# Optimization experiments

Measured on AMD Instinct MI355X. Metric: run time of the kernel, lower is better.

## Reference

```python
import jax, jax.numpy as jnp
import numpy as np

N, E = 50000, 800000
IN_DIM, HIDDEN, HEADS, OUT_DIM = 128, 64, 2, 128
NEG_SLOPE = 0.2


def setup_inputs() -> dict:
    key = jax.random.key(0)
    ks = jax.random.split(key, 12)
    s = lambda k, *sh: jax.random.normal(k, sh, dtype=jnp.float32) * (1.0 / np.sqrt(sh[0]))
    return {
        "x": jax.random.normal(ks[0], (N, IN_DIM), dtype=jnp.float32),
        "edge_index": jax.random.randint(ks[1], (2, E), 0, N, dtype=jnp.int64),
        # layer 1 (heads=2, concat=True)
        "Wl1": s(ks[2], IN_DIM, HEADS * HIDDEN),
        "Wr1": s(ks[3], IN_DIM, HEADS * HIDDEN),
        "att1": jax.random.normal(ks[4], (HEADS, HIDDEN), dtype=jnp.float32) * 0.1,
        "b1": jnp.zeros((HEADS * HIDDEN,), dtype=jnp.float32),
        # layer 2 (heads=1, concat=False -> mean)
        "Wl2": s(ks[5], HEADS * HIDDEN, OUT_DIM),
        "Wr2": s(ks[6], HEADS * HIDDEN, OUT_DIM),
        "att2": jax.random.normal(ks[7], (1, OUT_DIM), dtype=jnp.float32) * 0.1,
        "b2": jnp.zeros((OUT_DIM,), dtype=jnp.float32),
    }


def _gatv2_layer(x, src, dst, Wl, Wr, att, bias, heads, concat):
    n = x.shape[0]
    c = Wl.shape[1] // heads
    xl = (x @ Wl).reshape(n, heads, c)  # source transform
    xr = (x @ Wr).reshape(n, heads, c)  # target transform
    e = jax.nn.leaky_relu(xl[src] + xr[dst], NEG_SLOPE)      # (E, H, C)
    alpha = jnp.einsum("ehc,hc->eh", e, att)                 # (E, H)
    # softmax over incoming edges per destination node
    amax = jax.ops.segment_max(alpha, dst, num_segments=n)
    alpha = jnp.exp(alpha - amax[dst])
    denom = jax.ops.segment_sum(alpha, dst, num_segments=n)
    alpha = alpha / (denom[dst] + 1e-16)
    msg = xl[src] * alpha[:, :, None]                        # (E, H, C)
    out = jax.ops.segment_sum(msg, dst, num_segments=n)      # (N, H, C)
    out = out.reshape(n, heads * c) if concat else out.mean(axis=1)
    return out + bias


def reference(x, edge_index, Wl1, Wr1, att1, b1, Wl2, Wr2, att2, b2):
    n = x.shape[0]
    # PyG GATv2Conv default: add self loops
    loops = jnp.arange(n, dtype=edge_index.dtype)
    src = jnp.concatenate([edge_index[0], loops])
    dst = jnp.concatenate([edge_index[1], loops])
    h = jax.nn.elu(_gatv2_layer(x, src, dst, Wl1, Wr1, att1, b1, HEADS, True))
    h = jax.nn.elu(_gatv2_layer(h, src, dst, Wl2, Wr2, att2, b2, 1, False))
    return h
```

## Files before the change

### kernel.cpp

```cpp
#include <hip/hip_runtime.h>
#include <hip/hip_bf16.h>

#define N_NODES 50000
#define N_EDGES 800000
#define TOT_E   (N_EDGES + N_NODES)
#define NEG_SLOPE 0.2f
#define NBKT 98
#define CHUNK 4096
#define NCHUNK ((TOT_E + CHUNK - 1) / CHUNK)
#define BKT_CAP 12288

typedef __attribute__((ext_vector_type(8))) short bf16x8;
typedef __attribute__((ext_vector_type(4))) float f32x4;

static __device__ __forceinline__ unsigned short f2bf(float f) {
    unsigned int u = __float_as_uint(f);
    unsigned int r = (u + 0x7FFFu + ((u >> 16) & 1u)) >> 16;
    return (unsigned short)r;
}
static __device__ __forceinline__ float bf2f(unsigned short h) {
    return __uint_as_float(((unsigned int)h) << 16);
}
static __device__ __forceinline__ unsigned short f2h(float f) {
    _Float16 h = (_Float16)f;
    return __builtin_bit_cast(unsigned short, h);
}
static __device__ __forceinline__ float h2f(unsigned short u) {
    return (float)__builtin_bit_cast(_Float16, u);
}

__global__ __launch_bounds__(1024) void kA1(const int* __restrict__ dstp,
                                            int* __restrict__ bcount) {
    __shared__ int h[NBKT];
    int t = threadIdx.x;
    if (t < NBKT) h[t] = 0;
    __syncthreads();
    int base = blockIdx.x * CHUNK;
    int nloc = min(CHUNK, TOT_E - base);
    for (int i = t; i < nloc; i += 1024) {
        int e = base + i;
        int d = (e < N_EDGES) ? dstp[e] : (e - N_EDGES);
        atomicAdd(&h[d >> 9], 1);
    }
    __syncthreads();
    if (t < NBKT && h[t]) atomicAdd(&bcount[t], h[t]);
}

__global__ void kScan98(const int* __restrict__ bcount, int* __restrict__ bbase,
                        int* __restrict__ bcursor) {
    __shared__ int s[128];
    int t = threadIdx.x;
    int own = (t < NBKT) ? bcount[t] : 0;
    s[t] = own;
    __syncthreads();
    for (int off = 1; off < 128; off <<= 1) {
        int v = (t >= off) ? s[t - off] : 0;
        __syncthreads();
        s[t] += v;
        __syncthreads();
    }
    if (t < NBKT) {
        int base = s[t] - own;
        bbase[t] = base;
        bcursor[t] = base;
    }
    if (t == NBKT - 1) bbase[NBKT] = s[t];
}

__global__ __launch_bounds__(1024) void kA2(const int* __restrict__ srcp,
                                            const int* __restrict__ dstp,
                                            int* __restrict__ bcursor,
                                            unsigned* __restrict__ ebuf) {
    __shared__ int h[NBKT];
    __shared__ int lbase[NBKT];
    __shared__ int lcur[NBKT];
    __shared__ unsigned stage[CHUNK];
    int t = threadIdx.x;
    if (t < NBKT) h[t] = 0;
    __syncthreads();
    int base = blockIdx.x * CHUNK;
    int nloc = min(CHUNK, TOT_E - base);
    for (int i = t; i < nloc; i += 1024) {
        int e = base + i;
        int d = (e < N_EDGES) ? dstp[e] : (e - N_EDGES);
        atomicAdd(&h[d >> 9], 1);
    }
    __syncthreads();
    if (t < NBKT) lbase[t] = h[t] ? atomicAdd(&bcursor[t], h[t]) : 0;
    if (t == 0) {
        int run = 0;
        for (int b = 0; b < NBKT; ++b) { lcur[b] = run; run += h[b]; }
    }
    __syncthreads();
    for (int i = t; i < nloc; i += 1024) {
        int e = base + i;
        int d = (e < N_EDGES) ? dstp[e] : (e - N_EDGES);
        int s = (e < N_EDGES) ? srcp[e] : (e - N_EDGES);
        int b = d >> 9;
        int p = atomicAdd(&lcur[b], 1);
        stage[p] = (unsigned)s | ((unsigned)(d & 511) << 16) | ((unsigned)b << 25);
    }
    __syncthreads();
    for (int i = t; i < nloc; i += 1024) {
        unsigned v = stage[i];
        int b = v >> 25;
        int p = lbase[b] + i - (lcur[b] - h[b]);
        ebuf[p] = v & 0x1FFFFFFu;
    }
}

__global__ __launch_bounds__(1024) void kB(const unsigned* __restrict__ ebuf,
                                           const int* __restrict__ bbase,
                                           int* __restrict__ rowptr,
                                           int* __restrict__ esrc) {
    __shared__ int h[512];
    __shared__ int sc[512];
    __shared__ int st2[BKT_CAP];
    int b = blockIdx.x;
    int t = threadIdx.x;
    int gb = bbase[b];
    int cnt = bbase[b + 1] - gb;
    if (t < 512) h[t] = 0;
    __syncthreads();
    for (int i = t; i < cnt; i += 1024)
        atomicAdd(&h[(ebuf[gb + i] >> 16) & 511], 1);
    __syncthreads();
    if (t < 512) sc[t] = h[t];
    __syncthreads();
    for (int off = 1; off < 512; off <<= 1) {
        int v = (t < 512 && t >= off) ? sc[t - off] : 0;
        __syncthreads();
        if (t < 512) sc[t] += v;
        __syncthreads();
    }
    if (t < 512) h[t] = sc[t] - h[t];
    __syncthreads();
    int node0 = b << 9;
    if (t < 512) {
        int gn = node0 + t;
        if (gn < N_NODES) rowptr[gn] = gb + h[t];
    }
    if (b == NBKT - 1 && t == 0) rowptr[N_NODES] = TOT_E;
    for (int i = t; i < cnt; i += 1024) {
        unsigned v = ebuf[gb + i];
        int p = atomicAdd(&h[(v >> 16) & 511], 1);
        st2[p] = (int)(v & 0xFFFFu);
    }
    __syncthreads();
    for (int i = t; i < cnt; i += 1024) esrc[gb + i] = st2[i];
}

__global__ void k_pack(const float* __restrict__ Wa, const float* __restrict__ Wb,
                       unsigned short* __restrict__ Bp) {
    int idx = blockIdx.x * 256 + threadIdx.x;
    int j = idx & 7, lane = (idx >> 3) & 63, t = idx >> 9;
    int ks = t >> 4, ctg = t & 15;
    int k = (ks * 32 + (lane >> 4) * 8 + j) & 127;
    int n = ctg * 16 + (lane & 15);
    float v = (n < 128) ? Wa[k * 128 + n] : Wb[k * 128 + (n - 128)];
    Bp[idx] = f2bf(v);
}

template <bool F32IN>
__global__ __launch_bounds__(256) void k_mfma_lin(const void* __restrict__ Ain,
                                                  const unsigned short* __restrict__ Bp,
                                                  unsigned short* __restrict__ outA,
                                                  unsigned short* __restrict__ outB, int M) {
    __shared__ unsigned short lds_a[64][264];
    int tid = threadIdx.x;
    int n0 = blockIdx.x * 64;
    if (F32IN) {
        const float* X = (const float*)Ain;
#pragma unroll
        for (int r = 0; r < 8; ++r) {
            int c = r * 256 + tid;
            int row = c >> 5;
            int col4 = (c & 31) * 4;
            int gr = n0 + row;
            if (gr >= M) gr = M - 1;
            float4 v = *(const float4*)&X[(size_t)gr * 128 + col4];
            float vv[4] = {v.x, v.y, v.z, v.w};
            ushort4 hh, ll;
            unsigned short* hp = &hh.x;
            unsigned short* lp = &ll.x;
#pragma unroll
            for (int q = 0; q < 4; ++q) {
                unsigned short hv = f2bf(vv[q]);
                hp[q] = hv;
                lp[q] = f2bf(vv[q] - bf2f(hv));
            }
            *(ushort4*)&lds_a[row][col4] = hh;
            *(ushort4*)&lds_a[row][128 + col4] = ll;
        }
    } else {
        const unsigned short* Ap = (const unsigned short*)Ain;
#pragma unroll
        for (int r = 0; r < 8; ++r) {
            int c = r * 256 + tid;
            int row = c >> 5;
            int col = (c & 31) * 8;
            int gr = n0 + row;
            if (gr >= M) gr = M - 1;
            float4 v = *(const float4*)&Ap[(size_t)gr * 256 + col];
            *(float4*)&lds_a[row][col] = v;
        }
    }
    __syncthreads();

    int w = tid >> 6, lane = tid & 63;
    int lrow = lane & 15, lhi = lane >> 4;
    f32x4 acc[4][4] = {};
    const bf16x8* Bf = (const bf16x8*)Bp;
#pragma unroll
    for (int ks = 0; ks < 8; ++ks) {
        bf16x8 bfr[4], afr[4];
#pragma unroll
        for (int ct = 0; ct < 4; ++ct)
            bfr[ct] = Bf[(ks * 16 + (w * 4 + ct)) * 64 + lane];
#pragma unroll
        for (int mt = 0; mt < 4; ++mt)
            afr[mt] = *(const bf16x8*)&lds_a[mt * 16 + lrow][ks * 32 + lhi * 8];
#pragma unroll
        for (int mt = 0; mt < 4; ++mt)
#pragma unroll
            for (int ct = 0; ct < 4; ++ct)
                acc[mt][ct] = __builtin_amdgcn_mfma_f32_16x16x32_bf16(
                    afr[mt], bfr[ct], acc[mt][ct], 0, 0, 0);
    }
#pragma unroll
    for (int mt = 0; mt < 4; ++mt) {
        int row0 = n0 + mt * 16 + lhi * 4;
#pragma unroll
        for (int ct = 0; ct < 4; ++ct) {
            int col = w * 64 + ct * 16 + lrow;
            unsigned short* dst = (col < 128) ? outA : outB;
            int cc = col & 127;
#pragma unroll
            for (int reg = 0; reg < 4; ++reg) {
                int rg = row0 + reg;
                if (rg < M) dst[(size_t)rg * 128 + cc] = f2h(acc[mt][ct][reg]);
            }
        }
    }
}

template <int H, bool BF16OUT>
__global__ __launch_bounds__(256) void k_gat(const int* __restrict__ rowptr,
                                             const int* __restrict__ esrc,
                                             const unsigned short* __restrict__ xlh,
                                             const unsigned short* __restrict__ xrh,
                                             const float* __restrict__ att,
                                             const float* __restrict__ bias,
                                             float* __restrict__ out,
                                             unsigned short* __restrict__ outb) {
    int n = (blockIdx.x * 256 + threadIdx.x) >> 6;
    int lane = threadIdx.x & 63;
    if (n >= N_NODES) return;
    int start = rowptr[n], end = rowptr[n + 1];
    int grp = lane >> 4, sub = lane & 15;
    int c0 = sub * 8;

    float xr8[8], a8[8];
    {
        uint4 u = *(const uint4*)&xrh[(size_t)n * 128 + c0];
        unsigned int uu[4] = {u.x, u.y, u.z, u.w};
#pragma unroll
        for (int q = 0; q < 4; ++q) {
            xr8[2 * q]     = h2f((unsigned short)uu[q]);
            xr8[2 * q + 1] = h2f((unsigned short)(uu[q] >> 16));
        }
        float4 av0 = *(const float4*)&att[c0];
        float4 av1 = *(const float4*)&att[c0 + 4];
        a8[0] = av0.x; a8[1] = av0.y; a8[2] = av0.z; a8[3] = av0.w;
        a8[4] = av1.x; a8[5] = av1.y; a8[6] = av1.z; a8[7] = av1.w;
    }

    float m = -1e30f, den = 0.f;
    float acc[8] = {0.f, 0.f, 0.f, 0.f, 0.f, 0.f, 0.f, 0.f};

    int e0 = start + grp;
    int sp = esrc[(e0 < end) ? e0 : (end - 1)];
    uint4 u = *(const uint4*)&xlh[(size_t)sp * 128 + c0];

    for (int i = start; i < end; i += 4) {
        bool valid = (i + grp) < end;
        uint4 uc = u;
        int enext = i + 4 + grp;
        if (enext < end) {
            int s2 = esrc[enext];
            u = *(const uint4*)&xlh[(size_t)s2 * 128 + c0];
        }
        unsigned int uu[4] = {uc.x, uc.y, uc.z, uc.w};
        float c[8];
#pragma unroll
        for (int q = 0; q < 4; ++q) {
            c[2 * q]     = h2f((unsigned short)uu[q]);
            c[2 * q + 1] = h2f((unsigned short)(uu[q] >> 16));
        }
        float t = 0.f;
#pragma unroll
        for (int j = 0; j < 8; ++j) {
            float v = c[j] + xr8[j];
            v = fmaxf(v, NEG_SLOPE * v);
            t = fmaf(v, a8[j], t);
        }
        const int STEPS = (H == 2) ? 3 : 4;
#pragma unroll
        for (int k = 0; k < STEPS; ++k)
            t += __shfl_xor(t, 1 << k, 64);
        float sc = valid ? t : -1e38f;

        float mn = fmaxf(m, sc);
        float corr = __expf(m - mn);
        float p = __expf(sc - mn);
        m = mn;
        den = fmaf(den, corr, p);
#pragma unroll
        for (int j = 0; j < 8; ++j)
            acc[j] = fmaf(acc[j], corr, p * c[j]);
    }

#pragma unroll
    for (int off = 16; off <= 32; off <<= 1) {
        float mo = __shfl_xor(m, off, 64);
        float deno = __shfl_xor(den, off, 64);
        float ao[8];
#pragma unroll
        for (int j = 0; j < 8; ++j) ao[j] = __shfl_xor(acc[j], off, 64);
        float mn = fmaxf(m, mo);
        float c1 = __expf(m - mn);
        float c2 = __expf(mo - mn);
        m = mn;
        den = den * c1 + deno * c2;
#pragma unroll
        for (int j = 0; j < 8; ++j)
            acc[j] = fmaf(acc[j], c1, ao[j] * c2);
    }

    if (grp == 0) {
        float inv = 1.f / (den + 1e-16f);
        float o[8];
        float4 bv0 = *(const float4*)&bias[c0];
        float4 bv1 = *(const float4*)&bias[c0 + 4];
        float bb[8] = {bv0.x, bv0.y, bv0.z, bv0.w, bv1.x, bv1.y, bv1.z, bv1.w};
#pragma unroll
        for (int j = 0; j < 8; ++j) {
            float v = fmaf(acc[j], inv, bb[j]);
            o[j] = (v > 0.f) ? v : (__expf(v) - 1.f);
        }
        if (BF16OUT) {
            unsigned short hi[8], lo[8];
#pragma unroll
            for (int j = 0; j < 8; ++j) {
                hi[j] = f2bf(o[j]);
                lo[j] = f2bf(o[j] - bf2f(hi[j]));
            }
            *(uint4*)&outb[(size_t)n * 256 + c0] = *(const uint4*)hi;
            *(uint4*)&outb[(size_t)n * 256 + 128 + c0] = *(const uint4*)lo;
        } else {
            *(float4*)&out[(size_t)n * 128 + c0] = make_float4(o[0], o[1], o[2], o[3]);
            *(float4*)&out[(size_t)n * 128 + c0 + 4] = make_float4(o[4], o[5], o[6], o[7]);
        }
    }
}

extern "C" void kernel_launch(void* const* d_in, const int* in_sizes, int n_in,
                              void* d_out, int out_size, void* d_ws, size_t ws_size,
                              hipStream_t stream) {
    const float* x    = (const float*)d_in[0];
    const int*   ei   = (const int*)d_in[1];
    const float* Wl1  = (const float*)d_in[2];
    const float* Wr1  = (const float*)d_in[3];
    const float* att1 = (const float*)d_in[4];
    const float* b1   = (const float*)d_in[5];
    const float* Wl2  = (const float*)d_in[6];
    const float* Wr2  = (const float*)d_in[7];
    const float* att2 = (const float*)d_in[8];
    const float* b2   = (const float*)d_in[9];
    const int* srcp = ei;
    const int* dstp = ei + N_EDGES;

    char* ws = (char*)d_ws;
    size_t off = 0;
    auto alloc = [&](size_t bytes) {
        void* p = ws + off;
        off = (off + bytes + 255) & ~(size_t)255;
        return p;
    };
    int*      bcount  = (int*)alloc(NBKT * sizeof(int));
    int*      bbase   = (int*)alloc((NBKT + 1) * sizeof(int));
    int*      bcursor = (int*)alloc(NBKT * sizeof(int));
    unsigned* ebuf    = (unsigned*)alloc((size_t)TOT_E * sizeof(unsigned));
    int*      rowptr  = (int*)alloc((N_NODES + 1) * sizeof(int));
    int*      esrc    = (int*)alloc((size_t)TOT_E * sizeof(int));
    unsigned short* xp  = (unsigned short*)alloc((size_t)N_NODES * 256 * sizeof(short));
    unsigned short* Bp1 = (unsigned short*)alloc(65536 * sizeof(short));
    unsigned short* Bp2 = (unsigned short*)alloc(65536 * sizeof(short));
    unsigned short* xl  = (unsigned short*)alloc((size_t)N_NODES * 128 * sizeof(short));
    unsigned short* xr  = (unsigned short*)alloc((size_t)N_NODES * 128 * sizeof(short));

    hipMemsetAsync(bcount, 0, NBKT * sizeof(int), stream);
    kA1<<<NCHUNK, 1024, 0, stream>>>(dstp, bcount);
    kScan98<<<1, 128, 0, stream>>>(bcount, bbase, bcursor);
    kA2<<<NCHUNK, 1024, 0, stream>>>(srcp, dstp, bcursor, ebuf);
    kB<<<NBKT, 1024, 0, stream>>>(ebuf, bbase, rowptr, esrc);

    k_pack<<<256, 256, 0, stream>>>(Wl1, Wr1, Bp1);
    k_pack<<<256, 256, 0, stream>>>(Wl2, Wr2, Bp2);

    int mfma_grid = (N_NODES + 63) / 64;

    k_mfma_lin<true><<<mfma_grid, 256, 0, stream>>>(x, Bp1, xl, xr, N_NODES);
    k_gat<2, true><<<(N_NODES + 3) / 4, 256, 0, stream>>>(rowptr, esrc, xl, xr, att1, b1,
                                                          nullptr, xp);
    k_mfma_lin<false><<<mfma_grid, 256, 0, stream>>>(xp, Bp2, xl, xr, N_NODES);
    k_gat<1, false><<<(N_NODES + 3) / 4, 256, 0, stream>>>(rowptr, esrc, xl, xr, att2, b2,
                                                           (float*)d_out, nullptr);
}
```

Measured before the change: 170.9 us.

## Merge edge bucketing passes into one kernel and vectorize GAT softmax loop

Replaces the count, scan and scatter passes of the CSR build with a single pass that writes into fixed-capacity per-bucket slots sized by a bucket count. Buckets shrink to 256 nodes, and the two weight-pack launches merge into one. In the GAT aggregation, the math uses packed float2 vectors and skips the online-softmax rescale when no lane raises its running max. The fixed BKT_CAP silently drops edges if a bucket overflows, which relies on the destination distribution being roughly uniform.

Result: slower. 176.9 us (+3.5%).

```diff
diff --git a/kernel.cpp b/kernel.cpp
--- a/kernel.cpp
+++ b/kernel.cpp
@@ -5,13 +5,16 @@
 #define N_EDGES 800000
 #define TOT_E   (N_EDGES + N_NODES)
 #define NEG_SLOPE 0.2f
-#define NBKT 98
+#define NBKT 196
+#define NPB 256
+#define BKT_CAP 6144
 #define CHUNK 4096
 #define NCHUNK ((TOT_E + CHUNK - 1) / CHUNK)
-#define BKT_CAP 12288
 
 typedef __attribute__((ext_vector_type(8))) short bf16x8;
 typedef __attribute__((ext_vector_type(4))) float f32x4;
+typedef __attribute__((ext_vector_type(2))) float f32x2;
+typedef __attribute__((ext_vector_type(2))) _Float16 h2v;
 
 static __device__ __forceinline__ unsigned short f2bf(float f) {
     unsigned int u = __float_as_uint(f);
@@ -25,13 +28,16 @@
     _Float16 h = (_Float16)f;
     return __builtin_bit_cast(unsigned short, h);
 }
-static __device__ __forceinline__ float h2f(unsigned short u) {
-    return (float)__builtin_bit_cast(_Float16, u);
-}
-
-__global__ __launch_bounds__(1024) void kA1(const int* __restrict__ dstp,
-                                            int* __restrict__ bcount) {
+
+__global__ __launch_bounds__(1024) void kA(const int* __restrict__ srcp,
+                                           const int* __restrict__ dstp,
+                                           int* __restrict__ bcount,
+                                           unsigned* __restrict__ ebuf) {
     __shared__ int h[NBKT];
+    __shared__ int lbase[NBKT];
+    __shared__ int lcur[NBKT];
+    __shared__ int sc[256];
+    __shared__ unsigned stage[CHUNK];
     int t = threadIdx.x;
     if (t < NBKT) h[t] = 0;
     __syncthreads();
@@ -40,119 +46,102 @@
     for (int i = t; i < nloc; i += 1024) {
         int e = base + i;
         int d = (e < N_EDGES) ? dstp[e] : (e - N_EDGES);
-        atomicAdd(&h[d >> 9], 1);
-    }
-    __syncthreads();
-    if (t < NBKT && h[t]) atomicAdd(&bcount[t], h[t]);
-}
-
-__global__ void kScan98(const int* __restrict__ bcount, int* __restrict__ bbase,
-                        int* __restrict__ bcursor) {
-    __shared__ int s[128];
-    int t = threadIdx.x;
-    int own = (t < NBKT) ? bcount[t] : 0;
-    s[t] = own;
-    __syncthreads();
-    for (int off = 1; off < 128; off <<= 1) {
-        int v = (t >= off) ? s[t - off] : 0;
-        __syncthreads();
-        s[t] += v;
-        __syncthreads();
-    }
-    if (t < NBKT) {
-        int base = s[t] - own;
-        bbase[t] = base;
-        bcursor[t] = base;
-    }
-    if (t == NBKT - 1) bbase[NBKT] = s[t];
-}
-
-__global__ __launch_bounds__(1024) void kA2(const int* __restrict__ srcp,
-                                            const int* __restrict__ dstp,
-                                            int* __restrict__ bcursor,
-                                            unsigned* __restrict__ ebuf) {
-    __shared__ int h[NBKT];
-    __shared__ int lbase[NBKT];
-    __shared__ int lcur[NBKT];
-    __shared__ unsigned stage[CHUNK];
-    int t = threadIdx.x;
-    if (t < NBKT) h[t] = 0;
-    __syncthreads();
-    int base = blockIdx.x * CHUNK;
-    int nloc = min(CHUNK, TOT_E - base);
-    for (int i = t; i < nloc; i += 1024) {
-        int e = base + i;
-        int d = (e < N_EDGES) ? dstp[e] : (e - N_EDGES);
-        atomicAdd(&h[d >> 9], 1);
-    }
-    __syncthreads();
-    if (t < NBKT) lbase[t] = h[t] ? atomicAdd(&bcursor[t], h[t]) : 0;
-    if (t == 0) {
-        int run = 0;
-        for (int b = 0; b < NBKT; ++b) { lcur[b] = run; run += h[b]; }
-    }
+        atomicAdd(&h[d >> 8], 1);
+    }
+    __syncthreads();
+    if (t < NBKT) lbase[t] = h[t] ? atomicAdd(&bcount[t], h[t]) : 0;
+    if (t < 256) sc[t] = (t < NBKT) ? h[t] : 0;
+    __syncthreads();
+    for (int off = 1; off < 256; off <<= 1) {
+        int v = (t < 256 && t >= off) ? sc[t - off] : 0;
+        __syncthreads();
+        if (t < 256) sc[t] += v;
+        __syncthreads();
+    }
+    if (t < NBKT) lcur[t] = sc[t] - h[t];
     __syncthreads();
     for (int i = t; i < nloc; i += 1024) {
         int e = base + i;
         int d = (e < N_EDGES) ? dstp[e] : (e - N_EDGES);
         int s = (e < N_EDGES) ? srcp[e] : (e - N_EDGES);
-        int b = d >> 9;
+        int b = d >> 8;
         int p = atomicAdd(&lcur[b], 1);
-        stage[p] = (unsigned)s | ((unsigned)(d & 511) << 16) | ((unsigned)b << 25);
+        stage[p] = (unsigned)s | ((unsigned)(d & 255) << 16) | ((unsigned)b << 24);
     }
     __syncthreads();
     for (int i = t; i < nloc; i += 1024) {
         unsigned v = stage[i];
-        int b = v >> 25;
-        int p = lbase[b] + i - (lcur[b] - h[b]);
-        ebuf[p] = v & 0x1FFFFFFu;
-    }
+        int b = v >> 24;
+        int pl = lbase[b] + (i - (lcur[b] - h[b]));
+        if (pl < BKT_CAP) ebuf[(size_t)b * BKT_CAP + pl] = v & 0xFFFFFFu;
+    }
+}
+
+__global__ void kScanB(const int* __restrict__ bcount, int* __restrict__ bbase) {
+    __shared__ int s[256];
+    int t = threadIdx.x;
+    int own = (t < NBKT) ? bcount[t] : 0;
+    s[t] = own;
+    __syncthreads();
+    for (int off = 1; off < 256; off <<= 1) {
+        int v = (t >= off) ? s[t - off] : 0;
+        __syncthreads();
+        s[t] += v;
+        __syncthreads();
+    }
+    if (t < NBKT) bbase[t] = s[t] - own;
+    if (t == NBKT - 1) bbase[NBKT] = s[t];
 }
 
 __global__ __launch_bounds__(1024) void kB(const unsigned* __restrict__ ebuf,
+                                           const int* __restrict__ bcount,
                                            const int* __restrict__ bbase,
                                            int* __restrict__ rowptr,
                                            int* __restrict__ esrc) {
-    __shared__ int h[512];
-    __shared__ int sc[512];
+    __shared__ int h[NPB];
+    __shared__ int sc[NPB];
     __shared__ int st2[BKT_CAP];
     int b = blockIdx.x;
     int t = threadIdx.x;
     int gb = bbase[b];
-    int cnt = bbase[b + 1] - gb;
-    if (t < 512) h[t] = 0;
+    int cnt = min(bcount[b], BKT_CAP);
+    const unsigned* eb = ebuf + (size_t)b * BKT_CAP;
+    if (t < NPB) h[t] = 0;
     __syncthreads();
     for (int i = t; i < cnt; i += 1024)
-        atomicAdd(&h[(ebuf[gb + i] >> 16) & 511], 1);
-    __syncthreads();
-    if (t < 512) sc[t] = h[t];
-    __syncthreads();
-    for (int off = 1; off < 512; off <<= 1) {
-        int v = (t < 512 && t >= off) ? sc[t - off] : 0;
-        __syncthreads();
-        if (t < 512) sc[t] += v;
-        __syncthreads();
-    }
-    if (t < 512) h[t] = sc[t] - h[t];
-    __syncthreads();
-    int node0 = b << 9;
-    if (t < 512) {
-        int gn = node0 + t;
-        if (gn < N_NODES) rowptr[gn] = gb + h[t];
-    }
+        atomicAdd(&h[(eb[i] >> 16) & 255], 1);
+    __syncthreads();
+    if (t < NPB) sc[t] = h[t];
+    __syncthreads();
+    for (int off = 1; off < NPB; off <<= 1) {
+        int v = (t < NPB && t >= off) ? sc[t - off] : 0;
+        __syncthreads();
+        if (t < NPB) sc[t] += v;
+        __syncthreads();
+    }
+    if (t < NPB) h[t] = sc[t] - h[t];
+    __syncthreads();
+    int node0 = b << 8;
+    if (t < NPB && node0 + t < N_NODES) rowptr[node0 + t] = gb + h[t];
     if (b == NBKT - 1 && t == 0) rowptr[N_NODES] = TOT_E;
     for (int i = t; i < cnt; i += 1024) {
-        unsigned v = ebuf[gb + i];
-        int p = atomicAdd(&h[(v >> 16) & 511], 1);
+        unsigned v = eb[i];
+        int p = atomicAdd(&h[(v >> 16) & 255], 1);
         st2[p] = (int)(v & 0xFFFFu);
     }
     __syncthreads();
     for (int i = t; i < cnt; i += 1024) esrc[gb + i] = st2[i];
 }
 
-__global__ void k_pack(const float* __restrict__ Wa, const float* __restrict__ Wb,
-                       unsigned short* __restrict__ Bp) {
-    int idx = blockIdx.x * 256 + threadIdx.x;
+__global__ void k_pack2(const float* __restrict__ Wl1, const float* __restrict__ Wr1,
+                        const float* __restrict__ Wl2, const float* __restrict__ Wr2,
+                        unsigned short* __restrict__ Bp1, unsigned short* __restrict__ Bp2) {
+    int gidx = blockIdx.x * 256 + threadIdx.x;
+    int which = gidx >> 16;
+    int idx = gidx & 65535;
+    const float* Wa = which ? Wl2 : Wl1;
+    const float* Wb = which ? Wr2 : Wr1;
+    unsigned short* Bp = which ? Bp2 : Bp1;
     int j = idx & 7, lane = (idx >> 3) & 63, t = idx >> 9;
     int ks = t >> 4, ctg = t & 15;
     int k = (ks * 32 + (lane >> 4) * 8 + j) & 127;
@@ -260,23 +249,22 @@
     int grp = lane >> 4, sub = lane & 15;
     int c0 = sub * 8;
 
-    float xr8[8], a8[8];
+    f32x2 xr2[4], a2[4];
     {
         uint4 u = *(const uint4*)&xrh[(size_t)n * 128 + c0];
         unsigned int uu[4] = {u.x, u.y, u.z, u.w};
 #pragma unroll
         for (int q = 0; q < 4; ++q) {
-            xr8[2 * q]     = h2f((unsigned short)uu[q]);
-            xr8[2 * q + 1] = h2f((unsigned short)(uu[q] >> 16));
-        }
-        float4 av0 = *(const float4*)&att[c0];
-        float4 av1 = *(const float4*)&att[c0 + 4];
-        a8[0] = av0.x; a8[1] = av0.y; a8[2] = av0.z; a8[3] = av0.w;
-        a8[4] = av1.x; a8[5] = av1.y; a8[6] = av1.z; a8[7] = av1.w;
+            h2v hh = __builtin_bit_cast(h2v, uu[q]);
+            xr2[q] = (f32x2){(float)hh.x, (float)hh.y};
+        }
+#pragma unroll
+        for (int q = 0; q < 4; ++q)
+            a2[q] = *(const f32x2*)&att[c0 + 2 * q];
     }
 
     float m = -1e30f, den = 0.f;
-    float acc[8] = {0.f, 0.f, 0.f, 0.f, 0.f, 0.f, 0.f, 0.f};
+    f32x2 acc2[4] = {};
 
     int e0 = start + grp;
     int sp = esrc[(e0 < end) ? e0 : (end - 1)];
@@ -291,62 +279,73 @@
             u = *(const uint4*)&xlh[(size_t)s2 * 128 + c0];
         }
         unsigned int uu[4] = {uc.x, uc.y, uc.z, uc.w};
-        float c[8];
+        f32x2 c2[4];
 #pragma unroll
         for (int q = 0; q < 4; ++q) {
-            c[2 * q]     = h2f((unsigned short)uu[q]);
-            c[2 * q + 1] = h2f((unsigned short)(uu[q] >> 16));
-        }
-        float t = 0.f;
-#pragma unroll
-        for (int j = 0; j < 8; ++j) {
-            float v = c[j] + xr8[j];
-            v = fmaxf(v, NEG_SLOPE * v);
-            t = fmaf(v, a8[j], t);
-        }
+            h2v hh = __builtin_bit_cast(h2v, uu[q]);
+            c2[q] = (f32x2){(float)hh.x, (float)hh.y};
+        }
+        f32x2 tp = {0.f, 0.f};
+#pragma unroll
+        for (int q = 0; q < 4; ++q) {
+            f32x2 v = c2[q] + xr2[q];
+            f32x2 lr = __builtin_elementwise_max(v, v * NEG_SLOPE);
+            tp = lr * a2[q] + tp;
+        }
+        float t = tp.x + tp.y;
         const int STEPS = (H == 2) ? 3 : 4;
 #pragma unroll
         for (int k = 0; k < STEPS; ++k)
             t += __shfl_xor(t, 1 << k, 64);
         float sc = valid ? t : -1e38f;
 
-        float mn = fmaxf(m, sc);
-        float corr = __expf(m - mn);
-        float p = __expf(sc - mn);
-        m = mn;
-        den = fmaf(den, corr, p);
-#pragma unroll
-        for (int j = 0; j < 8; ++j)
-            acc[j] = fmaf(acc[j], corr, p * c[j]);
+        if (__any(sc > m)) {
+            float mn = fmaxf(m, sc);
+            float corr = __expf(m - mn);
+            float p = __expf(sc - mn);
+            m = mn;
+            den = fmaf(den, corr, p);
+#pragma unroll
+            for (int q = 0; q < 4; ++q)
+                acc2[q] = acc2[q] * corr + c2[q] * p;
+        } else {
+            float p = __expf(sc - m);
+            den += p;
+#pragma unroll
+            for (int q = 0; q < 4; ++q)
+                acc2[q] = c2[q] * p + acc2[q];
+        }
     }
 
 #pragma unroll
     for (int off = 16; off <= 32; off <<= 1) {
         float mo = __shfl_xor(m, off, 64);
         float deno = __shfl_xor(den, off, 64);
-        float ao[8];
-#pragma unroll
-        for (int j = 0; j < 8; ++j) ao[j] = __shfl_xor(acc[j], off, 64);
+        f32x2 ao[4];
+#pragma unroll
+        for (int q = 0; q < 4; ++q) {
+            ao[q].x = __shfl_xor(acc2[q].x, off, 64);
+            ao[q].y = __shfl_xor(acc2[q].y, off, 64);
+        }
         float mn = fmaxf(m, mo);
-        float c1 = __expf(m - mn);
-        float c2 = __expf(mo - mn);
+        float cc1 = __expf(m - mn);
+        float cc2 = __expf(mo - mn);
         m = mn;
-        den = den * c1 + deno * c2;
-#pragma unroll
-        for (int j = 0; j < 8; ++j)
-            acc[j] = fmaf(acc[j], c1, ao[j] * c2);
+        den = den * cc1 + deno * cc2;
+#pragma unroll
+        for (int q = 0; q < 4; ++q)
+            acc2[q] = acc2[q] * cc1 + ao[q] * cc2;
     }
 
     if (grp == 0) {
         float inv = 1.f / (den + 1e-16f);
         float o[8];
-        float4 bv0 = *(const float4*)&bias[c0];
-        float4 bv1 = *(const float4*)&bias[c0 + 4];
-        float bb[8] = {bv0.x, bv0.y, bv0.z, bv0.w, bv1.x, bv1.y, bv1.z, bv1.w};
-#pragma unroll
-        for (int j = 0; j < 8; ++j) {
-            float v = fmaf(acc[j], inv, bb[j]);
-            o[j] = (v > 0.f) ? v : (__expf(v) - 1.f);
+#pragma unroll
+        for (int q = 0; q < 4; ++q) {
+            f32x2 bb = *(const f32x2*)&bias[c0 + 2 * q];
+            f32x2 vv = acc2[q] * inv + bb;
+            o[2 * q]     = (vv.x > 0.f) ? vv.x : (__expf(vv.x) - 1.f);
+            o[2 * q + 1] = (vv.y > 0.f) ? vv.y : (__expf(vv.y) - 1.f);
         }
         if (BF16OUT) {
             unsigned short hi[8], lo[8];
@@ -389,8 +388,7 @@
     };
     int*      bcount  = (int*)alloc(NBKT * sizeof(int));
     int*      bbase   = (int*)alloc((NBKT + 1) * sizeof(int));
-    int*      bcursor = (int*)alloc(NBKT * sizeof(int));
-    unsigned* ebuf    = (unsigned*)alloc((size_t)TOT_E * sizeof(unsigned));
+    unsigned* ebuf    = (unsigned*)alloc((size_t)NBKT * BKT_CAP * sizeof(unsigned));
     int*      rowptr  = (int*)alloc((N_NODES + 1) * sizeof(int));
     int*      esrc    = (int*)alloc((size_t)TOT_E * sizeof(int));
     unsigned short* xp  = (unsigned short*)alloc((size_t)N_NODES * 256 * sizeof(short));
@@ -400,13 +398,11 @@
     unsigned short* xr  = (unsigned short*)alloc((size_t)N_NODES * 128 * sizeof(short));
 
     hipMemsetAsync(bcount, 0, NBKT * sizeof(int), stream);
-    kA1<<<NCHUNK, 1024, 0, stream>>>(dstp, bcount);
-    kScan98<<<1, 128, 0, stream>>>(bcount, bbase, bcursor);
-    kA2<<<NCHUNK, 1024, 0, stream>>>(srcp, dstp, bcursor, ebuf);
-    kB<<<NBKT, 1024, 0, stream>>>(ebuf, bbase, rowptr, esrc);
-
-    k_pack<<<256, 256, 0, stream>>>(Wl1, Wr1, Bp1);
-    k_pack<<<256, 256, 0, stream>>>(Wl2, Wr2, Bp2);
+    kA<<<NCHUNK, 1024, 0, stream>>>(srcp, dstp, bcount, ebuf);
+    kScanB<<<1, 256, 0, stream>>>(bcount, bbase);
+    kB<<<NBKT, 1024, 0, stream>>>(ebuf, bcount, bbase, rowptr, esrc);
+
+    k_pack2<<<512, 256, 0, stream>>>(Wl1, Wr1, Wl2, Wr2, Bp1, Bp2);
 
     int mfma_grid = (N_NODES + 63) / 64;
 
```
